# Kernel tuning notes

Measured on AMD Instinct MI355X. Metric: run time of the kernel, lower is better.

The kernel has to match this reference:

```python
import jax, jax.numpy as jnp
import numpy as np

B, C_CLS, D_WORD, J = 1024, 80, 300, 8000
IMG_CH = 2048

def setup_inputs() -> dict:
    key = jax.random.key(0)
    ks = jax.random.split(key, 9)
    return {
        'feature': jax.random.normal(ks[0], (B, IMG_CH), jnp.float32),
        'inp': jax.random.normal(ks[1], (1, C_CLS, D_WORD), jnp.float32),
        'A': jax.random.uniform(ks[2], (C_CLS, C_CLS), jnp.float32),
        'W_gc1': jax.random.normal(ks[3], (D_WORD, 1024), jnp.float32) * (1.0 / np.sqrt(1024)),
        'W_gc2': jax.random.normal(ks[4], (1024, 2048), jnp.float32) * (1.0 / np.sqrt(2048)),
        'W_img': jax.random.normal(ks[5], (J, IMG_CH), jnp.float32) * 0.02,
        'b_img': jax.random.normal(ks[6], (J,), jnp.float32) * 0.02,
        'W_cls': jax.random.normal(ks[7], (J, 2048), jnp.float32) * 0.02,
        'b_cls': jax.random.normal(ks[8], (J,), jnp.float32) * 0.02,
    }

def _gen_adj(A):
    # torch: D = A.sum(1)**-0.5; adj = (A @ diag(D)).T @ diag(D) = D[:,None]*A.T*D[None,:]
    D = jnp.power(jnp.sum(A, axis=1), -0.5)
    return D[:, None] * A.T * D[None, :]

def reference(feature, inp, A, W_gc1, W_gc2, W_img, b_img, W_cls, b_cls):
    inp0 = inp[0]                                   # [C, 300]
    adj = jax.lax.stop_gradient(_gen_adj(A))        # [C, C], .detach() in torch
    x = adj @ (inp0 @ W_gc1)                        # gc1: [C, 1024]
    x = jax.nn.leaky_relu(x, negative_slope=0.2)
    x = adj @ (x @ W_gc2)                           # gc2: [C, 2048]
    # MFB bilinear pooling (is_usemfb=True, is_hash=False -> out_in_tmp=1, eval-mode dropout=identity)
    # original: out[b,c] = sum_j (Linear_img(feature[b])[j] * Linear_cls(x_col_c)[j])
    img_proj = feature @ W_img.T + b_img            # [B, J]
    cls_proj = x @ W_cls.T + b_cls                  # [C, J]
    x_out = img_proj @ cls_proj.T                   # [B, C]
    return x_out
```

## Files before the change

kernel.cpp:

```cpp
#include <hip/hip_runtime.h>
#include <hip/hip_bf16.h>


typedef __bf16 bf16_t;
typedef __bf16 bf16x8 __attribute__((ext_vector_type(8)));
typedef float f32x4 __attribute__((ext_vector_type(4)));

#define MFMA16(a, b, c) __builtin_amdgcn_mfma_f32_16x16x32_bf16((a), (b), (c), 0, 0, 0)

__device__ inline bf16x8 cvt8(float4 a, float4 b) {
  bf16x8 v;
  v[0] = (bf16_t)a.x; v[1] = (bf16_t)a.y; v[2] = (bf16_t)a.z; v[3] = (bf16_t)a.w;
  v[4] = (bf16_t)b.x; v[5] = (bf16_t)b.y; v[6] = (bf16_t)b.z; v[7] = (bf16_t)b.w;
  return v;
}

__global__ void k_adj(const float* __restrict__ A, float* __restrict__ adj) {
  __shared__ float Dv[80];
  int tid = threadIdx.x;
  if (tid < 80) {
    float s = 0.f;
    #pragma unroll 4
    for (int j = 0; j < 80; ++j) s += A[tid * 80 + j];
    Dv[tid] = rsqrtf(s);
  }
  __syncthreads();
  for (int idx = tid; idx < 6400; idx += blockDim.x) {
    int i = idx / 80, j = idx % 80;
    adj[idx] = Dv[i] * Dv[j] * A[j * 80 + i];
  }
}

__global__ void k_cvt0(const float* __restrict__ inp0, bf16_t* __restrict__ x0b) {
  int idx = blockIdx.x * blockDim.x + threadIdx.x;
  if (idx < 30720) {
    int c = idx / 384, k = idx % 384;
    x0b[idx] = (k < 300) ? (bf16_t)inp0[c * 300 + k] : (bf16_t)0.f;
  }
}

__global__ __launch_bounds__(256) void k_gc1m(
    const bf16_t* __restrict__ x0b, const float* __restrict__ Wgc1,
    float* __restrict__ t1) {
  int tid = threadIdx.x;
  int w = tid >> 6, l = tid & 63;
  int ln = l & 15, q = l >> 4;
  int n0 = blockIdx.x * 16;

  __shared__ float red[4][80][16];
  f32x4 acc[5] = {};
  for (int ks = 0; ks < 3; ++ks) {
    int kq = w * 96 + ks * 32 + q * 8;
    bf16x8 bfrag;
    #pragma unroll
    for (int jj = 0; jj < 8; ++jj) {
      int k = kq + jj;
      int kc = k < 300 ? k : 299;
      float wv = Wgc1[kc * 1024 + n0 + ln];
      bfrag[jj] = (bf16_t)(k < 300 ? wv : 0.f);
    }
    #pragma unroll
    for (int mt = 0; mt < 5; ++mt) {
      bf16x8 afrag = *(const bf16x8*)(x0b + (size_t)(mt * 16 + ln) * 384 + kq);
      acc[mt] = MFMA16(afrag, bfrag, acc[mt]);
    }
  }
  #pragma unroll
  for (int mt = 0; mt < 5; ++mt)
    #pragma unroll
    for (int reg = 0; reg < 4; ++reg)
      red[w][mt * 16 + q * 4 + reg][ln] = acc[mt][reg];
  __syncthreads();
  for (int o = tid; o < 1280; o += 256) {
    int c = o >> 4, nn = o & 15;
    t1[c * 1024 + n0 + nn] = red[0][c][nn] + red[1][c][nn] + red[2][c][nn] + red[3][c][nn];
  }
}

__global__ void k_adjmul_leaky(const float* __restrict__ adj, const float* __restrict__ t1,
                               bf16_t* __restrict__ x1b) {
  int idx = blockIdx.x * blockDim.x + threadIdx.x;
  int c = idx >> 10, n = idx & 1023;
  const float* ar = adj + c * 80;
  float acc = 0.f;
  #pragma unroll 4
  for (int cc = 0; cc < 80; ++cc) acc += ar[cc] * t1[cc * 1024 + n];
  x1b[idx] = (bf16_t)(acc > 0.f ? acc : 0.2f * acc);
}

__global__ __launch_bounds__(256) void k_gc2m(
    const bf16_t* __restrict__ x1b, const float* __restrict__ Wgc2,
    float* __restrict__ t2) {
  int tid = threadIdx.x;
  int w = tid >> 6, l = tid & 63;
  int ln = l & 15, q = l >> 4;
  int n0 = blockIdx.x * 16;

  __shared__ float red[4][80][16];
  f32x4 acc[5] = {};
  for (int ks = 0; ks < 8; ++ks) {
    int kq = w * 256 + ks * 32 + q * 8;
    const float* bp = Wgc2 + (size_t)kq * 2048 + n0 + ln;
    bf16x8 bfrag;
    #pragma unroll
    for (int jj = 0; jj < 8; ++jj) bfrag[jj] = (bf16_t)bp[(size_t)jj * 2048];
    #pragma unroll
    for (int mt = 0; mt < 5; ++mt) {
      bf16x8 afrag = *(const bf16x8*)(x1b + (size_t)(mt * 16 + ln) * 1024 + kq);
      acc[mt] = MFMA16(afrag, bfrag, acc[mt]);
    }
  }
  #pragma unroll
  for (int mt = 0; mt < 5; ++mt)
    #pragma unroll
    for (int reg = 0; reg < 4; ++reg)
      red[w][mt * 16 + q * 4 + reg][ln] = acc[mt][reg];
  __syncthreads();
  for (int o = tid; o < 1280; o += 256) {
    int c = o >> 4, nn = o & 15;
    t2[c * 2048 + n0 + nn] = red[0][c][nn] + red[1][c][nn] + red[2][c][nn] + red[3][c][nn];
  }
}

__global__ void k_adjmul_bf16(const float* __restrict__ adj, const float* __restrict__ t2,
                              bf16_t* __restrict__ x2) {
  int idx = blockIdx.x * blockDim.x + threadIdx.x;
  int c = idx >> 11, n = idx & 2047;
  const float* ar = adj + c * 80;
  float acc = 0.f;
  #pragma unroll 4
  for (int cc = 0; cc < 80; ++cc) acc += ar[cc] * t2[cc * 2048 + n];
  x2[idx] = (bf16_t)acc;
}

__global__ __launch_bounds__(256) void k_clsproj(
    const float* __restrict__ Wcls, const float* __restrict__ bcls,
    const float* __restrict__ bimg, const bf16_t* __restrict__ x2,
    bf16_t* __restrict__ P, float* __restrict__ r) {
  int tid = threadIdx.x;
  int w = tid >> 6, l = tid & 63;
  int ln = l & 15, q = l >> 4;
  int j0 = blockIdx.x * 16;
  size_t jrow = (size_t)(j0 + ln) * 2048;

  __shared__ float red[4][80][16];
  __shared__ float rloc[80];
  if (tid < 80) rloc[tid] = 0.f;

  f32x4 acc[5] = {};
  int kbase = w * 512 + q * 8;
  for (int ks = 0; ks < 16; ++ks) {
    int kq = kbase + ks * 32;
    const float4* bp = (const float4*)(Wcls + jrow + kq);
    float4 b0 = bp[0], b1 = bp[1];
    bf16x8 bfrag = cvt8(b0, b1);
    #pragma unroll
    for (int mt = 0; mt < 5; ++mt) {
      bf16x8 afrag = *(const bf16x8*)(x2 + (size_t)(mt * 16 + ln) * 2048 + kq);
      acc[mt] = MFMA16(afrag, bfrag, acc[mt]);
    }
  }
  #pragma unroll
  for (int mt = 0; mt < 5; ++mt)
    #pragma unroll
    for (int reg = 0; reg < 4; ++reg)
      red[w][mt * 16 + q * 4 + reg][ln] = acc[mt][reg];
  __syncthreads();

  for (int o = tid; o < 1280; o += 256) {
    int c = o >> 4, jj = o & 15;
    float v = red[0][c][jj] + red[1][c][jj] + red[2][c][jj] + red[3][c][jj] + bcls[j0 + jj];
    P[(size_t)c * 8000 + j0 + jj] = (bf16_t)v;
    atomicAdd(&rloc[c], bimg[j0 + jj] * v);
  }
  __syncthreads();
  if (tid < 80) atomicAdd(&r[tid], rloc[tid]);
}

__global__ __launch_bounds__(256) void k_hmat(
    const float* __restrict__ Wimg, const bf16_t* __restrict__ P, float* __restrict__ H) {
  int tid = threadIdx.x;
  int w = tid >> 6, l = tid & 63;
  int ln = l & 15, q = l >> 4;
  int nc = blockIdx.x & 31, jc = blockIdx.x >> 5;
  int col = nc * 64 + w * 16 + ln;

  f32x4 acc[5] = {};
  int jbase = jc * 800 + q * 8;
  for (int ks = 0; ks < 25; ++ks) {
    int jq = jbase + ks * 32;
    const float* bp = Wimg + (size_t)jq * 2048 + col;
    bf16x8 bfrag;
    #pragma unroll
    for (int jj = 0; jj < 8; ++jj) bfrag[jj] = (bf16_t)bp[(size_t)jj * 2048];
    #pragma unroll
    for (int mt = 0; mt < 5; ++mt) {
      bf16x8 afrag = *(const bf16x8*)(P + (size_t)(mt * 16 + ln) * 8000 + jq);
      acc[mt] = MFMA16(afrag, bfrag, acc[mt]);
    }
  }
  #pragma unroll
  for (int mt = 0; mt < 5; ++mt)
    #pragma unroll
    for (int reg = 0; reg < 4; ++reg)
      atomicAdd(&H[(size_t)(mt * 16 + q * 4 + reg) * 2048 + col], acc[mt][reg]);
}

__global__ __launch_bounds__(256) void k_out(
    const float* __restrict__ feat, const float* __restrict__ H,
    const float* __restrict__ r, float* __restrict__ out) {
  int tid = threadIdx.x;
  int w = tid >> 6, l = tid & 63;
  int ln = l & 15, q = l >> 4;
  int mg = blockIdx.x & 15, kc = blockIdx.x >> 4;
  int m0 = mg * 64 + w * 16;
  size_t frow = (size_t)(m0 + ln) * 2048;

  f32x4 acc[5] = {};
  int kbase = kc * 256 + q * 8;
  for (int ks = 0; ks < 8; ++ks) {
    int kq = kbase + ks * 32;
    const float4* ap = (const float4*)(feat + frow + kq);
    bf16x8 afrag = cvt8(ap[0], ap[1]);
    #pragma unroll
    for (int nt = 0; nt < 5; ++nt) {
      const float4* hp = (const float4*)(H + (size_t)(nt * 16 + ln) * 2048 + kq);
      bf16x8 bfrag = cvt8(hp[0], hp[1]);
      acc[nt] = MFMA16(afrag, bfrag, acc[nt]);
    }
  }
  #pragma unroll
  for (int nt = 0; nt < 5; ++nt)
    #pragma unroll
    for (int reg = 0; reg < 4; ++reg) {
      int b = m0 + q * 4 + reg;
      int c = nt * 16 + ln;
      float v = acc[nt][reg];
      if (kc == 0) v += r[c];
      atomicAdd(&out[b * 80 + c], v);
    }
}

extern "C" void kernel_launch(void* const* d_in, const int* in_sizes, int n_in,
                              void* d_out, int out_size, void* d_ws, size_t ws_size,
                              hipStream_t stream) {
  const float* feature = (const float*)d_in[0];
  const float* inp     = (const float*)d_in[1];
  const float* A       = (const float*)d_in[2];
  const float* Wgc1    = (const float*)d_in[3];
  const float* Wgc2    = (const float*)d_in[4];
  const float* Wimg    = (const float*)d_in[5];
  const float* bimg    = (const float*)d_in[6];
  const float* Wcls    = (const float*)d_in[7];
  const float* bcls    = (const float*)d_in[8];
  float* out = (float*)d_out;

  char* ws = (char*)d_ws;
  float*  adj = (float*)(ws + 0);
  float*  t1  = (float*)(ws + 25600);
  bf16_t* x1b = (bf16_t*)(ws + 353280);
  float*  t2  = (float*)(ws + 517120);
  bf16_t* x2  = (bf16_t*)(ws + 1172480);
  bf16_t* P   = (bf16_t*)(ws + 1500160);
  float*  H   = (float*)(ws + 2780160);
  float*  r   = (float*)(ws + 3435520);
  bf16_t* x0b = (bf16_t*)(ws + 3435840);

  hipMemsetAsync(H, 0, 80 * 2048 * 4, stream);
  hipMemsetAsync(r, 0, 80 * 4, stream);
  hipMemsetAsync(out, 0, 1024 * 80 * 4, stream);

  k_adj<<<1, 128, 0, stream>>>(A, adj);
  k_cvt0<<<120, 256, 0, stream>>>(inp, x0b);
  k_gc1m<<<64, 256, 0, stream>>>(x0b, Wgc1, t1);
  k_adjmul_leaky<<<320, 256, 0, stream>>>(adj, t1, x1b);
  k_gc2m<<<128, 256, 0, stream>>>(x1b, Wgc2, t2);
  k_adjmul_bf16<<<640, 256, 0, stream>>>(adj, t2, x2);
  k_clsproj<<<500, 256, 0, stream>>>(Wcls, bcls, bimg, x2, P, r);
  k_hmat<<<320, 256, 0, stream>>>(Wimg, P, H);
  k_out<<<128, 256, 0, stream>>>(feature, H, r, out);
}
```

Before: 289.9 us.

## Stage weight tiles through LDS with coalesced float4 loads and finer split-K

k_gc2m and k_hmat now load the fp32 weight tiles (Wgc2, Wimg) into shared memory with coalesced float4 reads, then build bf16 B fragments from LDS. Before, each lane did strided scalar global loads. Both kernels also split K more finely, giving more blocks (512 and 800), and reduce partial results with atomicAdd, so t2 needs an extra memset. This is meant to fix uncoalesced weight reads and poor occupancy, at the cost of extra atomics and per-stage syncthreads.

```diff
diff --git a/kernel.cpp b/kernel.cpp
--- a/kernel.cpp
+++ b/kernel.cpp
@@ -94,32 +94,36 @@
   int tid = threadIdx.x;
   int w = tid >> 6, l = tid & 63;
   int ln = l & 15, q = l >> 4;
-  int n0 = blockIdx.x * 16;
-
-  __shared__ float red[4][80][16];
-  f32x4 acc[5] = {};
-  for (int ks = 0; ks < 8; ++ks) {
-    int kq = w * 256 + ks * 32 + q * 8;
-    const float* bp = Wgc2 + (size_t)kq * 2048 + n0 + ln;
+  int nc = blockIdx.x & 31, kc = blockIdx.x >> 5;
+
+  __shared__ float Bs[32][66];
+  f32x4 acc[5] = {};
+  for (int s = 0; s < 2; ++s) {
+    int k0 = kc * 64 + s * 32;
+    #pragma unroll
+    for (int it = 0; it < 2; ++it) {
+      int slot = tid + it * 256;
+      int kr = slot >> 4, nq = slot & 15;
+      const float4 v = *(const float4*)(Wgc2 + (size_t)(k0 + kr) * 2048 + nc * 64 + nq * 4);
+      *(float4*)&Bs[kr][nq * 4] = v;
+    }
+    __syncthreads();
     bf16x8 bfrag;
     #pragma unroll
-    for (int jj = 0; jj < 8; ++jj) bfrag[jj] = (bf16_t)bp[(size_t)jj * 2048];
-    #pragma unroll
-    for (int mt = 0; mt < 5; ++mt) {
-      bf16x8 afrag = *(const bf16x8*)(x1b + (size_t)(mt * 16 + ln) * 1024 + kq);
-      acc[mt] = MFMA16(afrag, bfrag, acc[mt]);
-    }
-  }
-  #pragma unroll
-  for (int mt = 0; mt < 5; ++mt)
-    #pragma unroll
-    for (int reg = 0; reg < 4; ++reg)
-      red[w][mt * 16 + q * 4 + reg][ln] = acc[mt][reg];
-  __syncthreads();
-  for (int o = tid; o < 1280; o += 256) {
-    int c = o >> 4, nn = o & 15;
-    t2[c * 2048 + n0 + nn] = red[0][c][nn] + red[1][c][nn] + red[2][c][nn] + red[3][c][nn];
-  }
+    for (int jj = 0; jj < 8; ++jj) bfrag[jj] = (bf16_t)Bs[q * 8 + jj][w * 16 + ln];
+    #pragma unroll
+    for (int mt = 0; mt < 5; ++mt) {
+      bf16x8 afrag = *(const bf16x8*)(x1b + (size_t)(mt * 16 + ln) * 1024 + k0 + q * 8);
+      acc[mt] = MFMA16(afrag, bfrag, acc[mt]);
+    }
+    __syncthreads();
+  }
+  #pragma unroll
+  for (int mt = 0; mt < 5; ++mt)
+    #pragma unroll
+    for (int reg = 0; reg < 4; ++reg)
+      atomicAdd(&t2[(size_t)(mt * 16 + q * 4 + reg) * 2048 + nc * 64 + w * 16 + ln],
+                acc[mt][reg]);
 }
 
 __global__ void k_adjmul_bf16(const float* __restrict__ adj, const float* __restrict__ t2,
@@ -183,27 +187,35 @@
   int w = tid >> 6, l = tid & 63;
   int ln = l & 15, q = l >> 4;
   int nc = blockIdx.x & 31, jc = blockIdx.x >> 5;
-  int col = nc * 64 + w * 16 + ln;
-
-  f32x4 acc[5] = {};
-  int jbase = jc * 800 + q * 8;
-  for (int ks = 0; ks < 25; ++ks) {
-    int jq = jbase + ks * 32;
-    const float* bp = Wimg + (size_t)jq * 2048 + col;
+
+  __shared__ float Bs[32][66];
+  f32x4 acc[5] = {};
+  for (int s = 0; s < 10; ++s) {
+    int j0 = jc * 320 + s * 32;
+    #pragma unroll
+    for (int it = 0; it < 2; ++it) {
+      int slot = tid + it * 256;
+      int jr = slot >> 4, nq = slot & 15;
+      const float4 v = *(const float4*)(Wimg + (size_t)(j0 + jr) * 2048 + nc * 64 + nq * 4);
+      *(float4*)&Bs[jr][nq * 4] = v;
+    }
+    __syncthreads();
     bf16x8 bfrag;
     #pragma unroll
-    for (int jj = 0; jj < 8; ++jj) bfrag[jj] = (bf16_t)bp[(size_t)jj * 2048];
-    #pragma unroll
-    for (int mt = 0; mt < 5; ++mt) {
-      bf16x8 afrag = *(const bf16x8*)(P + (size_t)(mt * 16 + ln) * 8000 + jq);
-      acc[mt] = MFMA16(afrag, bfrag, acc[mt]);
-    }
-  }
-  #pragma unroll
-  for (int mt = 0; mt < 5; ++mt)
-    #pragma unroll
-    for (int reg = 0; reg < 4; ++reg)
-      atomicAdd(&H[(size_t)(mt * 16 + q * 4 + reg) * 2048 + col], acc[mt][reg]);
+    for (int jj = 0; jj < 8; ++jj) bfrag[jj] = (bf16_t)Bs[q * 8 + jj][w * 16 + ln];
+    #pragma unroll
+    for (int mt = 0; mt < 5; ++mt) {
+      bf16x8 afrag = *(const bf16x8*)(P + (size_t)(mt * 16 + ln) * 8000 + j0 + q * 8);
+      acc[mt] = MFMA16(afrag, bfrag, acc[mt]);
+    }
+    __syncthreads();
+  }
+  #pragma unroll
+  for (int mt = 0; mt < 5; ++mt)
+    #pragma unroll
+    for (int reg = 0; reg < 4; ++reg)
+      atomicAdd(&H[(size_t)(mt * 16 + q * 4 + reg) * 2048 + nc * 64 + w * 16 + ln],
+                acc[mt][reg]);
 }
 
 __global__ __launch_bounds__(256) void k_out(
@@ -266,6 +278,7 @@
   float*  r   = (float*)(ws + 3435520);
   bf16_t* x0b = (bf16_t*)(ws + 3435840);
 
+  hipMemsetAsync(t2, 0, 80 * 2048 * 4, stream);
   hipMemsetAsync(H, 0, 80 * 2048 * 4, stream);
   hipMemsetAsync(r, 0, 80 * 4, stream);
   hipMemsetAsync(out, 0, 1024 * 80 * 4, stream);
@@ -274,9 +287,9 @@
   k_cvt0<<<120, 256, 0, stream>>>(inp, x0b);
   k_gc1m<<<64, 256, 0, stream>>>(x0b, Wgc1, t1);
   k_adjmul_leaky<<<320, 256, 0, stream>>>(adj, t1, x1b);
-  k_gc2m<<<128, 256, 0, stream>>>(x1b, Wgc2, t2);
+  k_gc2m<<<512, 256, 0, stream>>>(x1b, Wgc2, t2);
   k_adjmul_bf16<<<640, 256, 0, stream>>>(adj, t2, x2);
   k_clsproj<<<500, 256, 0, stream>>>(Wcls, bcls, bimg, x2, P, r);
-  k_hmat<<<320, 256, 0, stream>>>(Wimg, P, H);
+  k_hmat<<<800, 256, 0, stream>>>(Wimg, P, H);
   k_out<<<128, 256, 0, stream>>>(feature, H, r, out);
 }
```

Result: faster. 282.0 us (-2.7%).
